# Performance work log

Measured on AMD Instinct MI355X. Metric: run time of the kernel, lower is better.

Reference implementation:

```python
import jax, jax.numpy as jnp
import numpy as np

H = 1024
V = 50257
L = 512


def setup_inputs() -> dict:
    key = jax.random.key(0)
    ks = jax.random.split(key, 12)
    s = 0.02
    return {
        "input_tok": jax.random.randint(ks[0], (1,), 0, V, dtype=jnp.int64),
        "hidden": jax.random.normal(ks[1], (1, 1, H), dtype=jnp.float32),
        "encoder_outputs": jax.random.normal(ks[2], (L, 1, H), dtype=jnp.float32),
        "embedding_w": jax.random.normal(ks[3], (V, H), dtype=jnp.float32) * s,
        "attn_combine_w": jax.random.normal(ks[4], (H, 2 * H), dtype=jnp.float32) * s,
        "attn_combine_b": jax.random.normal(ks[5], (H,), dtype=jnp.float32) * s,
        "w_ih": jax.random.normal(ks[6], (3 * H, H), dtype=jnp.float32) * s,
        "w_hh": jax.random.normal(ks[7], (3 * H, H), dtype=jnp.float32) * s,
        "b_ih": jax.random.normal(ks[8], (3 * H,), dtype=jnp.float32) * s,
        "b_hh": jax.random.normal(ks[9], (3 * H,), dtype=jnp.float32) * s,
        "out_w": jax.random.normal(ks[10], (V, H), dtype=jnp.float32) * s,
        "out_b": jax.random.normal(ks[11], (V,), dtype=jnp.float32) * s,
    }


def reference(input_tok, hidden, encoder_outputs, embedding_w,
              attn_combine_w, attn_combine_b, w_ih, w_hh, b_ih, b_hh,
              out_w, out_b):
    # embedding(input).view(1,1,-1); dropout is identity in eval mode
    embedded = embedding_w[input_tok[0]][None, :]          # [1, H]
    enc = encoder_outputs[:, 0, :]                          # [L, H]
    h0 = hidden[0]                                          # [1, H]
    # dot-product attention: hidden[0] @ enc^T
    attn_weights = jax.nn.softmax(h0 @ enc.T, axis=1)      # [1, L]
    attn_applied = attn_weights @ enc                       # [1, H]
    combined = jnp.concatenate([embedded, attn_applied], axis=1)  # [1, 2H]
    x = jax.nn.relu(combined @ attn_combine_w.T + attn_combine_b)  # [1, H]
    # single-step GRU cell (PyTorch gate ordering: r, z, n)
    gi = x @ w_ih.T + b_ih                                  # [1, 3H]
    gh = h0 @ w_hh.T + b_hh                                 # [1, 3H]
    r = jax.nn.sigmoid(gi[:, :H] + gh[:, :H])
    z = jax.nn.sigmoid(gi[:, H:2 * H] + gh[:, H:2 * H])
    n = jnp.tanh(gi[:, 2 * H:] + r * gh[:, 2 * H:])
    h_new = (1.0 - z) * n + z * h0                          # [1, H]
    logp = jax.nn.log_softmax(h_new @ out_w.T + out_b, axis=1)  # [1, V]
    return logp, h_new[None], attn_weights
```

## Files before the change

kernel.cpp:

```cpp
#include <hip/hip_runtime.h>
#include <math.h>

#define H  1024
#define H2 2048
#define V  50257
#define L  512
#define NL 3142

__device__ __forceinline__ float dot4(float4 a, float4 b) {
    return a.x*b.x + a.y*b.y + a.z*b.z + a.w*b.w;
}
__device__ __forceinline__ float wave_red_sum(float v) {
    #pragma unroll
    for (int off = 32; off > 0; off >>= 1) v += __shfl_down(v, off, 64);
    return v;
}
__device__ __forceinline__ float wave_red_max(float v) {
    #pragma unroll
    for (int off = 32; off > 0; off >>= 1) v = fmaxf(v, __shfl_down(v, off, 64));
    return v;
}

__global__ void __launch_bounds__(256) k_scores(
        const float* __restrict__ h0, const float* __restrict__ enc,
        float* __restrict__ scores) {
    __shared__ float sred[4];
    int t = threadIdx.x, lane = t & 63, wv = t >> 6;
    int l = blockIdx.x;
    float4 a = ((const float4*)(enc + (size_t)l * H))[t];
    float4 b = ((const float4*)h0)[t];
    float acc = wave_red_sum(dot4(a, b));
    if (lane == 0) sred[wv] = acc;
    __syncthreads();
    if (t == 0) scores[l] = sred[0] + sred[1] + sred[2] + sred[3];
}

__global__ void __launch_bounds__(256) k_attn(
        const float* __restrict__ enc, const float* __restrict__ scores,
        float* __restrict__ attn, float* __restrict__ d_out) {
    __shared__ float wl[L];
    __shared__ float sred[4];
    int t = threadIdx.x, lane = t & 63, wv = t >> 6;
    float s0 = scores[t], s1 = scores[t + 256];
    float m = wave_red_max(fmaxf(s0, s1));
    if (lane == 0) sred[wv] = m;
    __syncthreads();
    float gmax = fmaxf(fmaxf(sred[0], sred[1]), fmaxf(sred[2], sred[3]));
    __syncthreads();
    float e0 = expf(s0 - gmax), e1 = expf(s1 - gmax);
    float ssum = wave_red_sum(e0 + e1);
    if (lane == 0) sred[wv] = ssum;
    __syncthreads();
    float inv = 1.f / (sred[0] + sred[1] + sred[2] + sred[3]);
    float w0 = e0 * inv, w1 = e1 * inv;
    wl[t] = w0; wl[t + 256] = w1;
    if (blockIdx.x == 0) {
        d_out[V + H + t]       = w0;
        d_out[V + H + 256 + t] = w1;
    }
    __syncthreads();
    int col = blockIdx.x * 4 + wv;
    float acc = 0.f;
    #pragma unroll
    for (int k = 0; k < 8; ++k)
        acc += wl[k * 64 + lane] * enc[(size_t)(k * 64 + lane) * H + col];
    acc = wave_red_sum(acc);
    if (lane == 0) attn[col] = acc;
}

__global__ void __launch_bounds__(256) k_combine(
        const float* __restrict__ emb_w, const int* __restrict__ tok,
        const float* __restrict__ attn, const float* __restrict__ Wc,
        const float* __restrict__ bc, float* __restrict__ x) {
    __shared__ float comb[H2];
    int t = threadIdx.x;
    int tk = tok[0];
    ((float4*)comb)[t]       = ((const float4*)(emb_w + (size_t)tk * H))[t];
    ((float4*)comb)[t + 256] = ((const float4*)attn)[t];
    __syncthreads();
    int lane = t & 63, wv = t >> 6;
    int row = blockIdx.x * 4 + wv;
    const float4* wr = (const float4*)(Wc + (size_t)row * H2);
    float acc = 0.f;
    #pragma unroll
    for (int j = 0; j < 8; ++j)
        acc += dot4(wr[j * 64 + lane], ((const float4*)comb)[j * 64 + lane]);
    acc = wave_red_sum(acc);
    if (lane == 0) x[row] = fmaxf(acc + bc[row], 0.f);
}

__global__ void __launch_bounds__(256, 4) k_gru(
        const float* __restrict__ x, const float* __restrict__ h0,
        const float* __restrict__ w_ih, const float* __restrict__ b_ih,
        const float* __restrict__ w_hh, const float* __restrict__ b_hh,
        float* __restrict__ d_out, float* __restrict__ hnew) {
    int t = threadIdx.x, lane = t & 63, wv = t >> 6;
    int i = blockIdx.x * 4 + wv;
    const float4* x4 = (const float4*)x;
    const float4* h4 = (const float4*)h0;
    float gi[3], gh[3];
    #pragma unroll
    for (int k = 0; k < 3; ++k) {
        const float4* wi = (const float4*)(w_ih + (size_t)(k * H + i) * H);
        const float4* wh = (const float4*)(w_hh + (size_t)(k * H + i) * H);
        float ai = 0.f, ah = 0.f;
        #pragma unroll
        for (int j = 0; j < 4; ++j) {
            ai += dot4(wi[j * 64 + lane], x4[j * 64 + lane]);
            ah += dot4(wh[j * 64 + lane], h4[j * 64 + lane]);
        }
        #pragma unroll
        for (int off = 32; off > 0; off >>= 1) {
            ai += __shfl_down(ai, off, 64);
            ah += __shfl_down(ah, off, 64);
        }
        gi[k] = ai; gh[k] = ah;
    }
    if (lane == 0) {
        float r = 1.f / (1.f + expf(-(gi[0] + b_ih[i]       + gh[0] + b_hh[i])));
        float z = 1.f / (1.f + expf(-(gi[1] + b_ih[H + i]   + gh[1] + b_hh[H + i])));
        float n = tanhf(gi[2] + b_ih[2 * H + i] + r * (gh[2] + b_hh[2 * H + i]));
        float h = (1.f - z) * n + z * h0[i];
        d_out[V + i] = h;
        hnew[i] = h;
    }
}

__global__ void __launch_bounds__(256, 4) k_logits(
        const float* __restrict__ hnew, const float* __restrict__ out_w,
        const float* __restrict__ out_b, float* __restrict__ d_out,
        float* __restrict__ pm, float* __restrict__ ps) {
    __shared__ float4 hs4[256];
    __shared__ float sm[4], ss[4];
    int t = threadIdx.x, lane = t & 63, wv = t >> 6;
    hs4[t] = ((const float4*)hnew)[t];
    __syncthreads();
    int base = blockIdx.x * 16 + wv * 4;
    const float4* wr[4];
    #pragma unroll
    for (int r = 0; r < 4; ++r) {
        int row = (base + r < V) ? base + r : V - 1;
        wr[r] = (const float4*)(out_w + (size_t)row * H);
    }
    float a[4] = {0.f, 0.f, 0.f, 0.f};
    #pragma unroll
    for (int j = 0; j < 4; ++j) {
        float4 hv = hs4[j * 64 + lane];
        #pragma unroll
        for (int r = 0; r < 4; ++r) a[r] += dot4(wr[r][j * 64 + lane], hv);
    }
    #pragma unroll
    for (int off = 32; off > 0; off >>= 1) {
        #pragma unroll
        for (int r = 0; r < 4; ++r) a[r] += __shfl_down(a[r], off, 64);
    }
    if (lane == 0) {
        float v[4];
        float m = -INFINITY;
        #pragma unroll
        for (int r = 0; r < 4; ++r) {
            int row = base + r;
            if (row < V) {
                v[r] = a[r] + out_b[row];
                d_out[row] = v[r];
                m = fmaxf(m, v[r]);
            } else v[r] = -INFINITY;
        }
        float s = 0.f;
        #pragma unroll
        for (int r = 0; r < 4; ++r)
            if (base + r < V) s += expf(v[r] - m);
        sm[wv] = m; ss[wv] = s;
    }
    __syncthreads();
    if (t == 0) {
        float M = fmaxf(fmaxf(sm[0], sm[1]), fmaxf(sm[2], sm[3]));
        float S = 0.f;
        #pragma unroll
        for (int k = 0; k < 4; ++k)
            if (sm[k] > -INFINITY) S += ss[k] * expf(sm[k] - M);
        pm[blockIdx.x] = M; ps[blockIdx.x] = S;
    }
}

__global__ void __launch_bounds__(256) k_logp(
        float* __restrict__ d_out, const float* __restrict__ pm,
        const float* __restrict__ ps) {
    __shared__ float sm[4], ss[4];
    int t = threadIdx.x, lane = t & 63, wv = t >> 6;
    float m = -INFINITY, s = 0.f;
    for (int i = t; i < NL; i += 256) {
        float mi = pm[i], si = ps[i];
        float mn = fmaxf(m, mi);
        s = s * expf(m - mn) + si * expf(mi - mn);
        m = mn;
    }
    #pragma unroll
    for (int off = 32; off > 0; off >>= 1) {
        float mo = __shfl_down(m, off, 64);
        float so = __shfl_down(s, off, 64);
        float mn = fmaxf(m, mo);
        s = s * expf(m - mn) + so * expf(mo - mn);
        m = mn;
    }
    if (lane == 0) { sm[wv] = m; ss[wv] = s; }
    __syncthreads();
    float M = fmaxf(fmaxf(sm[0], sm[1]), fmaxf(sm[2], sm[3]));
    float S = 0.f;
    #pragma unroll
    for (int k = 0; k < 4; ++k) S += ss[k] * expf(sm[k] - M);
    float off = M + logf(S);
    int i = blockIdx.x * 256 + t;
    if (i < V) d_out[i] -= off;
}

extern "C" void kernel_launch(void* const* d_in, const int* in_sizes, int n_in,
                              void* d_out, int out_size, void* d_ws, size_t ws_size,
                              hipStream_t stream) {
    const int*   tok    = (const int*)d_in[0];
    const float* hidden = (const float*)d_in[1];
    const float* enc    = (const float*)d_in[2];
    const float* emb_w  = (const float*)d_in[3];
    const float* Wc     = (const float*)d_in[4];
    const float* bc     = (const float*)d_in[5];
    const float* w_ih   = (const float*)d_in[6];
    const float* w_hh   = (const float*)d_in[7];
    const float* b_ih   = (const float*)d_in[8];
    const float* b_hh   = (const float*)d_in[9];
    const float* out_w  = (const float*)d_in[10];
    const float* out_b  = (const float*)d_in[11];
    float* out = (float*)d_out;
    float* ws  = (float*)d_ws;

    float* scores = ws;
    float* attn   = ws + 4096;
    float* xbuf   = ws + 5120;
    float* hnew   = ws + 6144;
    float* pm     = ws + 8192;
    float* psum   = ws + 12288;

    k_scores <<<512, 256, 0, stream>>>(hidden, enc, scores);
    k_attn   <<<256, 256, 0, stream>>>(enc, scores, attn, out);
    k_combine<<<256, 256, 0, stream>>>(emb_w, tok, attn, Wc, bc, xbuf);
    k_gru    <<<256, 256, 0, stream>>>(xbuf, hidden, w_ih, b_ih, w_hh, b_hh, out, hnew);
    k_logits <<<NL,  256, 0, stream>>>(hnew, out_w, out_b, out, pm, psum);
    k_logp   <<<(V + 255) / 256, 256, 0, stream>>>(out, pm, psum);
}
```

Measured before the change: 423.8 us.

## Split attention-apply into row-partial blocks and merge six GRU dot products

Replaces the column-strided attention-apply kernel, whose loads were uncoalesced and which launched 256 blocks each rereading the scores, with 16 blocks. Each block reads 32 encoder rows coalesced as float4 and writes a partial sum, and the combine kernel reduces those 16 partials. The GRU kernel now issues all six row dot products in one loop, sharing the x/h loads, and drops the occupancy hint. The logits kernel reads the hidden vector straight from global memory instead of staging it in LDS behind a barrier. The cost is an extra partial buffer and a redundant 16-way partial reduction in every combine block.

```diff
diff --git a/kernel.cpp b/kernel.cpp
--- a/kernel.cpp
+++ b/kernel.cpp
@@ -1,11 +1,12 @@
 #include <hip/hip_runtime.h>
 #include <math.h>
 
-#define H  1024
-#define H2 2048
-#define V  50257
-#define L  512
-#define NL 3142
+#define H   1024
+#define H2  2048
+#define V   50257
+#define L   512
+#define NL  3142
+#define NAB 16
 
 __device__ __forceinline__ float dot4(float4 a, float4 b) {
     return a.x*b.x + a.y*b.y + a.z*b.z + a.w*b.w;
@@ -35,9 +36,9 @@
     if (t == 0) scores[l] = sred[0] + sred[1] + sred[2] + sred[3];
 }
 
-__global__ void __launch_bounds__(256) k_attn(
+__global__ void __launch_bounds__(256) k_attn_part(
         const float* __restrict__ enc, const float* __restrict__ scores,
-        float* __restrict__ attn, float* __restrict__ d_out) {
+        float* __restrict__ partial, float* __restrict__ d_out) {
     __shared__ float wl[L];
     __shared__ float sred[4];
     int t = threadIdx.x, lane = t & 63, wv = t >> 6;
@@ -59,24 +60,32 @@
         d_out[V + H + 256 + t] = w1;
     }
     __syncthreads();
-    int col = blockIdx.x * 4 + wv;
-    float acc = 0.f;
-    #pragma unroll
-    for (int k = 0; k < 8; ++k)
-        acc += wl[k * 64 + lane] * enc[(size_t)(k * 64 + lane) * H + col];
-    acc = wave_red_sum(acc);
-    if (lane == 0) attn[col] = acc;
+    int r0 = blockIdx.x * 32;
+    float4 acc = make_float4(0.f, 0.f, 0.f, 0.f);
+    #pragma unroll 8
+    for (int k = 0; k < 32; ++k) {
+        float w  = wl[r0 + k];
+        float4 e = ((const float4*)(enc + (size_t)(r0 + k) * H))[t];
+        acc.x += w * e.x; acc.y += w * e.y; acc.z += w * e.z; acc.w += w * e.w;
+    }
+    ((float4*)(partial + (size_t)blockIdx.x * H))[t] = acc;
 }
 
 __global__ void __launch_bounds__(256) k_combine(
         const float* __restrict__ emb_w, const int* __restrict__ tok,
-        const float* __restrict__ attn, const float* __restrict__ Wc,
+        const float* __restrict__ partial, const float* __restrict__ Wc,
         const float* __restrict__ bc, float* __restrict__ x) {
     __shared__ float comb[H2];
     int t = threadIdx.x;
+    float4 a = make_float4(0.f, 0.f, 0.f, 0.f);
+    #pragma unroll
+    for (int b = 0; b < NAB; ++b) {
+        float4 p = ((const float4*)(partial + (size_t)b * H))[t];
+        a.x += p.x; a.y += p.y; a.z += p.z; a.w += p.w;
+    }
     int tk = tok[0];
     ((float4*)comb)[t]       = ((const float4*)(emb_w + (size_t)tk * H))[t];
-    ((float4*)comb)[t + 256] = ((const float4*)attn)[t];
+    ((float4*)comb)[t + 256] = a;
     __syncthreads();
     int lane = t & 63, wv = t >> 6;
     int row = blockIdx.x * 4 + wv;
@@ -89,7 +98,7 @@
     if (lane == 0) x[row] = fmaxf(acc + bc[row], 0.f);
 }
 
-__global__ void __launch_bounds__(256, 4) k_gru(
+__global__ void __launch_bounds__(256) k_gru(
         const float* __restrict__ x, const float* __restrict__ h0,
         const float* __restrict__ w_ih, const float* __restrict__ b_ih,
         const float* __restrict__ w_hh, const float* __restrict__ b_hh,
@@ -98,28 +107,37 @@
     int i = blockIdx.x * 4 + wv;
     const float4* x4 = (const float4*)x;
     const float4* h4 = (const float4*)h0;
-    float gi[3], gh[3];
-    #pragma unroll
-    for (int k = 0; k < 3; ++k) {
-        const float4* wi = (const float4*)(w_ih + (size_t)(k * H + i) * H);
-        const float4* wh = (const float4*)(w_hh + (size_t)(k * H + i) * H);
-        float ai = 0.f, ah = 0.f;
-        #pragma unroll
-        for (int j = 0; j < 4; ++j) {
-            ai += dot4(wi[j * 64 + lane], x4[j * 64 + lane]);
-            ah += dot4(wh[j * 64 + lane], h4[j * 64 + lane]);
-        }
-        #pragma unroll
-        for (int off = 32; off > 0; off >>= 1) {
-            ai += __shfl_down(ai, off, 64);
-            ah += __shfl_down(ah, off, 64);
-        }
-        gi[k] = ai; gh[k] = ah;
+    const float4* wi0 = (const float4*)(w_ih + (size_t)i * H);
+    const float4* wi1 = (const float4*)(w_ih + (size_t)(H + i) * H);
+    const float4* wi2 = (const float4*)(w_ih + (size_t)(2 * H + i) * H);
+    const float4* wh0 = (const float4*)(w_hh + (size_t)i * H);
+    const float4* wh1 = (const float4*)(w_hh + (size_t)(H + i) * H);
+    const float4* wh2 = (const float4*)(w_hh + (size_t)(2 * H + i) * H);
+    float ai0 = 0.f, ai1 = 0.f, ai2 = 0.f, ah0 = 0.f, ah1 = 0.f, ah2 = 0.f;
+    #pragma unroll
+    for (int j = 0; j < 4; ++j) {
+        int idx = j * 64 + lane;
+        float4 xv = x4[idx], hv = h4[idx];
+        ai0 += dot4(wi0[idx], xv);
+        ai1 += dot4(wi1[idx], xv);
+        ai2 += dot4(wi2[idx], xv);
+        ah0 += dot4(wh0[idx], hv);
+        ah1 += dot4(wh1[idx], hv);
+        ah2 += dot4(wh2[idx], hv);
+    }
+    #pragma unroll
+    for (int off = 32; off > 0; off >>= 1) {
+        ai0 += __shfl_down(ai0, off, 64);
+        ai1 += __shfl_down(ai1, off, 64);
+        ai2 += __shfl_down(ai2, off, 64);
+        ah0 += __shfl_down(ah0, off, 64);
+        ah1 += __shfl_down(ah1, off, 64);
+        ah2 += __shfl_down(ah2, off, 64);
     }
     if (lane == 0) {
-        float r = 1.f / (1.f + expf(-(gi[0] + b_ih[i]       + gh[0] + b_hh[i])));
-        float z = 1.f / (1.f + expf(-(gi[1] + b_ih[H + i]   + gh[1] + b_hh[H + i])));
-        float n = tanhf(gi[2] + b_ih[2 * H + i] + r * (gh[2] + b_hh[2 * H + i]));
+        float r = 1.f / (1.f + expf(-(ai0 + b_ih[i]         + ah0 + b_hh[i])));
+        float z = 1.f / (1.f + expf(-(ai1 + b_ih[H + i]     + ah1 + b_hh[H + i])));
+        float n = tanhf(ai2 + b_ih[2 * H + i] + r * (ah2 + b_hh[2 * H + i]));
         float h = (1.f - z) * n + z * h0[i];
         d_out[V + i] = h;
         hnew[i] = h;
@@ -130,12 +148,10 @@
         const float* __restrict__ hnew, const float* __restrict__ out_w,
         const float* __restrict__ out_b, float* __restrict__ d_out,
         float* __restrict__ pm, float* __restrict__ ps) {
-    __shared__ float4 hs4[256];
     __shared__ float sm[4], ss[4];
     int t = threadIdx.x, lane = t & 63, wv = t >> 6;
-    hs4[t] = ((const float4*)hnew)[t];
-    __syncthreads();
     int base = blockIdx.x * 16 + wv * 4;
+    const float4* h4 = (const float4*)hnew;
     const float4* wr[4];
     #pragma unroll
     for (int r = 0; r < 4; ++r) {
@@ -145,7 +161,7 @@
     float a[4] = {0.f, 0.f, 0.f, 0.f};
     #pragma unroll
     for (int j = 0; j < 4; ++j) {
-        float4 hv = hs4[j * 64 + lane];
+        float4 hv = h4[j * 64 + lane];
         #pragma unroll
         for (int r = 0; r < 4; ++r) a[r] += dot4(wr[r][j * 64 + lane], hv);
     }
@@ -232,17 +248,17 @@
     float* out = (float*)d_out;
     float* ws  = (float*)d_ws;
 
-    float* scores = ws;
-    float* attn   = ws + 4096;
-    float* xbuf   = ws + 5120;
-    float* hnew   = ws + 6144;
-    float* pm     = ws + 8192;
-    float* psum   = ws + 12288;
-
-    k_scores <<<512, 256, 0, stream>>>(hidden, enc, scores);
-    k_attn   <<<256, 256, 0, stream>>>(enc, scores, attn, out);
-    k_combine<<<256, 256, 0, stream>>>(emb_w, tok, attn, Wc, bc, xbuf);
-    k_gru    <<<256, 256, 0, stream>>>(xbuf, hidden, w_ih, b_ih, w_hh, b_hh, out, hnew);
-    k_logits <<<NL,  256, 0, stream>>>(hnew, out_w, out_b, out, pm, psum);
-    k_logp   <<<(V + 255) / 256, 256, 0, stream>>>(out, pm, psum);
-}
+    float* scores  = ws;
+    float* partial = ws + 1024;
+    float* xbuf    = ws + 17408;
+    float* hnew    = ws + 18432;
+    float* pm      = ws + 19456;
+    float* psum    = ws + 23040;
+
+    k_scores   <<<512, 256, 0, stream>>>(hidden, enc, scores);
+    k_attn_part<<<NAB, 256, 0, stream>>>(enc, scores, partial, out);
+    k_combine  <<<256, 256, 0, stream>>>(emb_w, tok, partial, Wc, bc, xbuf);
+    k_gru      <<<256, 256, 0, stream>>>(xbuf, hidden, w_ih, b_ih, w_hh, b_hh, out, hnew);
+    k_logits   <<<NL,  256, 0, stream>>>(hnew, out_w, out_b, out, pm, psum);
+    k_logp     <<<(V + 255) / 256, 256, 0, stream>>>(out, pm, psum);
+}
```

Result: no change. 420.7 us (-0.7%).
